# Kernel tuning notes

Measured on AMD Instinct MI355X. Metric: run time of the kernel, lower is better.

Reference implementation:

```python
import jax, jax.numpy as jnp
import numpy as np

N, E, H, D_IN, D_OUT, DEPTH, G = 100000, 1600000, 128, 128, 10, 3, 256


def setup_inputs() -> dict:
    key = jax.random.key(0)
    ks = jax.random.split(key, 16)
    s = lambda k, shape: jax.random.normal(k, shape, dtype=jnp.float32) * 0.05
    inp = {
        "x": jax.random.normal(ks[0], (N, D_IN), dtype=jnp.float32),
        "edge_index": jax.random.randint(ks[1], (2, E), 0, N, dtype=jnp.int32),
        "control_edge_index": jax.random.randint(ks[2], (2, 1024), 0, N, dtype=jnp.int32),
        "batch": jnp.sort(jax.random.randint(ks[3], (N,), 0, G, dtype=jnp.int32)),
        # encoder MLP: input_dim -> hidden -> hidden
        "enc_w1": s(ks[4], (D_IN, H)), "enc_b1": jnp.zeros((H,), jnp.float32),
        "enc_w2": s(ks[5], (H, H)),    "enc_b2": jnp.zeros((H,), jnp.float32),
        # conv_depth GCN layers, hidden -> hidden
        "conv_w": s(ks[6], (DEPTH, H, H)), "conv_b": jnp.zeros((DEPTH, H), jnp.float32),
        # decoder MLP: hidden -> hidden -> output_dim
        "dec_w1": s(ks[7], (H, H)),     "dec_b1": jnp.zeros((H,), jnp.float32),
        "dec_w2": s(ks[8], (H, D_OUT)), "dec_b2": jnp.zeros((D_OUT,), jnp.float32),
    }
    return inp


def _gcn_forward(x, enc_w1, enc_b1, enc_w2, enc_b2, conv_w, conv_b,
                 dec_w1, dec_b1, dec_w2, dec_b2, edge_index, batch):
    # encoder MLP (Linear-ReLU-Dropout(eval)-Linear)
    h = jax.nn.relu(x @ enc_w1 + enc_b1) @ enc_w2 + enc_b2

    # GCN normalization with self-loops: D^{-1/2} (A + I) D^{-1/2}
    loops = jnp.arange(N, dtype=edge_index.dtype)
    src = jnp.concatenate([edge_index[0], loops])  # [E + N]
    dst = jnp.concatenate([edge_index[1], loops])
    deg = jax.ops.segment_sum(jnp.ones_like(src, dtype=h.dtype), dst, num_segments=N)
    inv_sqrt = jax.lax.rsqrt(deg)  # deg >= 1 thanks to self-loops
    coef = (inv_sqrt[src] * inv_sqrt[dst])[:, None]  # [E+N, 1]

    for l in range(DEPTH):
        hw = h @ conv_w[l] + conv_b[l]                      # [N, H]
        h = jax.ops.segment_sum(hw[src] * coef, dst, num_segments=N)
        if l < DEPTH - 1:  # linear=False -> nonlinearity between convs
            h = jax.nn.relu(h)

    # global_add_pool over graph ids
    pooled = jax.ops.segment_sum(h, batch, num_segments=G)   # [G, H]

    # decoder MLP
    return jax.nn.relu(pooled @ dec_w1 + dec_b1) @ dec_w2 + dec_b2  # [G, D_OUT]


def reference(x, edge_index, control_edge_index, batch, enc_w1, enc_b1, enc_w2,
              enc_b2, conv_w, conv_b, dec_w1, dec_b1, dec_w2, dec_b2):
    # control_edge_index corresponds to the (disabled) control mechanism; unused
    return _gcn_forward(x, enc_w1, enc_b1, enc_w2, enc_b2, conv_w, conv_b,
                        dec_w1, dec_b1, dec_w2, dec_b2, edge_index, batch)
```

## Files before the change

### kernel.cpp

```cpp
#include <hip/hip_runtime.h>
#include <hip/hip_bf16.h>
#include <cstdint>
#include <cstddef>

#define NN 100000
#define NE 1600000
#define HH 128
#define NG 256

#define NB 196
#define BSH 9
#define BMSK 511
#define CHUNK 4096
#define NBLK 391
#define GB 782
#define NBK 391

typedef __bf16 bf16x8 __attribute__((ext_vector_type(8)));
typedef float floatx4 __attribute__((ext_vector_type(4)));

__device__ __forceinline__ uint32_t f2b(float f) {
  union { float f; uint32_t u; } v; v.f = f;
  uint32_t u = v.u;
  return (u + 0x7FFFu + ((u >> 16) & 1u)) >> 16;
}
__device__ __forceinline__ float blo(uint32_t u) {
  union { uint32_t u; float f; } v; v.u = u << 16;
  return v.f;
}
__device__ __forceinline__ float bhi(uint32_t u) {
  union { uint32_t u; float f; } v; v.u = u & 0xFFFF0000u;
  return v.f;
}
__device__ __forceinline__ void addrow(float* a, uint4 v) {
  a[0] += blo(v.x); a[1] += bhi(v.x);
  a[2] += blo(v.y); a[3] += bhi(v.y);
  a[4] += blo(v.z); a[5] += bhi(v.z);
  a[6] += blo(v.w); a[7] += bhi(v.w);
}

__device__ __forceinline__ void stage_w(uint16_t (*Wt)[136], const float* __restrict__ W,
                                        int tid) {
  for (int it = 0; it < 16; ++it) {
    int idx = tid + it * 256;
    int n = idx & 127;
    int k0 = (idx >> 7) * 4;
    uint2 wv;
    wv.x = f2b(W[(k0 + 0) * 128 + n]) | (f2b(W[(k0 + 1) * 128 + n]) << 16);
    wv.y = f2b(W[(k0 + 2) * 128 + n]) | (f2b(W[(k0 + 3) * 128 + n]) << 16);
    *(uint2*)&Wt[n][k0] = wv;
  }
}

__global__ __launch_bounds__(256) void k_front(const int* __restrict__ src,
                                               int* __restrict__ blkcnt,
                                               const float* __restrict__ conv_w,
                                               uint16_t* __restrict__ wbf,
                                               float* __restrict__ pooled) {
  int t = threadIdx.x;
  if (blockIdx.x < NBLK) {
    __shared__ int h[NB];
    if (t < NB) h[t] = 0;
    __syncthreads();
    int base = blockIdx.x * CHUNK, end = min(base + CHUNK, NE);
    for (int i = base + t; i < end; i += 256) atomicAdd(&h[src[i] >> BSH], 1);
    __syncthreads();
    if (t < NB) blkcnt[blockIdx.x * NB + t] = h[t];
  } else if (blockIdx.x < NBLK + 128) {
    int idx = (blockIdx.x - NBLK) * 256 + t;
    int l = idx >> 14;
    int n = (idx >> 7) & 127;
    int k = idx & 127;
    wbf[idx] = (uint16_t)f2b(conv_w[(l + 1) * 16384 + k * 128 + n]);
  } else {
    int i = ((blockIdx.x - NBLK - 128) * 256 + t) * 4;
    if (i < NG * HH) *(float4*)&pooled[i] = make_float4(0.f, 0.f, 0.f, 0.f);
  }
}

__global__ __launch_bounds__(256) void k_cntB(const uint2* __restrict__ pairs,
                                              int* __restrict__ blkcnt) {
  __shared__ int h[NB];
  int t = threadIdx.x;
  if (t < NB) h[t] = 0;
  __syncthreads();
  int base = blockIdx.x * CHUNK, end = min(base + CHUNK, NE);
  for (int i = base + t; i < end; i += 256) atomicAdd(&h[pairs[i].y >> BSH], 1);
  __syncthreads();
  if (t < NB) blkcnt[blockIdx.x * NB + t] = h[t];
}

__global__ void k_scan(const int* __restrict__ blkcnt, int* __restrict__ poff,
                       int* __restrict__ gbase, int* __restrict__ off, int set_off) {
  __shared__ int s[256];
  int t = threadIdx.x;
  int tot = 0;
  if (t < NB) {
    for (int r = 0; r < NBLK; ++r) {
      poff[r * NB + t] = tot;
      tot += blkcnt[r * NB + t];
    }
  }
  s[t] = (t < NB) ? tot : 0;
  __syncthreads();
  for (int d = 1; d < 256; d <<= 1) {
    int v = (t >= d) ? s[t - d] : 0;
    __syncthreads();
    s[t] += v;
    __syncthreads();
  }
  if (t < NB) gbase[t] = s[t] - tot;
  if (t == 0) { gbase[NB] = NE; if (set_off) off[NN] = NE; }
}

__global__ __launch_bounds__(256) void k_placeA(const int* __restrict__ src,
                                                const int* __restrict__ dst,
                                                const int* __restrict__ poff,
                                                const int* __restrict__ gbase,
                                                uint2* __restrict__ pairs) {
  __shared__ int cur[NB];
  int t = threadIdx.x;
  if (t < NB) cur[t] = poff[blockIdx.x * NB + t] + gbase[t];
  __syncthreads();
  int base = blockIdx.x * CHUNK, end = min(base + CHUNK, NE);
  for (int i = base + t; i < end; i += 256) {
    int s = src[i], d = dst[i];
    int p = atomicAdd(&cur[s >> BSH], 1);
    pairs[p] = make_uint2((unsigned)s, (unsigned)d);
  }
}

__global__ __launch_bounds__(256) void k_placeB(const uint2* __restrict__ pairs,
                                                const int* __restrict__ poff,
                                                const int* __restrict__ gbase,
                                                uint32_t* __restrict__ outb) {
  __shared__ int cur[NB];
  int t = threadIdx.x;
  if (t < NB) cur[t] = poff[blockIdx.x * NB + t] + gbase[t];
  __syncthreads();
  int base = blockIdx.x * CHUNK, end = min(base + CHUNK, NE);
  for (int i = base + t; i < end; i += 256) {
    uint2 v = pairs[i];
    int p = atomicAdd(&cur[v.y >> BSH], 1);
    outb[p] = v.x | ((v.y & (unsigned)BMSK) << 17);
  }
}

__global__ __launch_bounds__(256) void k_sortenc(
    const uint32_t* __restrict__ pairbuf, const int* __restrict__ gbase,
    const int* __restrict__ batch,
    int* __restrict__ off, int* __restrict__ csrs,
    int* __restrict__ dhist2, int* __restrict__ gstart,
    const float* __restrict__ A32, const float* __restrict__ W,
    const float* __restrict__ bias, uint16_t* __restrict__ Out)
{
  __shared__ char smraw[34816];
  const int tid = threadIdx.x;

  if (blockIdx.x < GB) {
    auto Wt = (uint16_t(*)[136])smraw;
    stage_w(Wt, W, tid);
    __syncthreads();

    const int lane = tid & 63;
    const int wave = tid >> 6;
    const int lrow = lane & 15;
    const int quad = lane >> 4;
    const int lk = quad * 8;
    const int row0 = blockIdx.x * 128 + wave * 32;

    floatx4 acc[2][8];
#pragma unroll
    for (int t = 0; t < 2; ++t)
#pragma unroll
      for (int n = 0; n < 8; ++n)
        acc[t][n] = (floatx4){0.f, 0.f, 0.f, 0.f};

#pragma unroll
    for (int ks = 0; ks < 4; ++ks) {
      bf16x8 a[2];
#pragma unroll
      for (int t = 0; t < 2; ++t) {
        int r = row0 + t * 16 + lrow;
        uint4 tmp = {0u, 0u, 0u, 0u};
        if (r < NN) {
          float4 f0 = *(const float4*)(A32 + (size_t)r * HH + ks * 32 + lk);
          float4 f1 = *(const float4*)(A32 + (size_t)r * HH + ks * 32 + lk + 4);
          tmp.x = f2b(f0.x) | (f2b(f0.y) << 16);
          tmp.y = f2b(f0.z) | (f2b(f0.w) << 16);
          tmp.z = f2b(f1.x) | (f2b(f1.y) << 16);
          tmp.w = f2b(f1.z) | (f2b(f1.w) << 16);
        }
        a[t] = __builtin_bit_cast(bf16x8, tmp);
      }
#pragma unroll
      for (int n = 0; n < 8; ++n) {
        bf16x8 b = __builtin_bit_cast(bf16x8, *(const uint4*)&Wt[n * 16 + lrow][ks * 32 + lk]);
        acc[0][n] = __builtin_amdgcn_mfma_f32_16x16x32_bf16(b, a[0], acc[0][n], 0, 0, 0);
        acc[1][n] = __builtin_amdgcn_mfma_f32_16x16x32_bf16(b, a[1], acc[1][n], 0, 0, 0);
      }
    }

    float4 b4[8];
#pragma unroll
    for (int n = 0; n < 8; ++n) b4[n] = *(const float4*)(bias + n * 16 + quad * 4);

#pragma unroll
    for (int t = 0; t < 2; ++t) {
      int row = row0 + t * 16 + lrow;
      if (row < NN) {
        uint16_t* orow = Out + (size_t)row * HH;
#pragma unroll
        for (int n = 0; n < 8; ++n) {
          float v0 = fmaxf(acc[t][n][0] + b4[n].x, 0.f);
          float v1 = fmaxf(acc[t][n][1] + b4[n].y, 0.f);
          float v2 = fmaxf(acc[t][n][2] + b4[n].z, 0.f);
          float v3 = fmaxf(acc[t][n][3] + b4[n].w, 0.f);
          uint2 o;
          o.x = f2b(v0) | (f2b(v1) << 16);
          o.y = f2b(v2) | (f2b(v3) << 16);
          *(uint2*)(orow + n * 16 + quad * 4) = o;
        }
      }
    }
  } else {
    int* cnt  = (int*)smraw;
    int* loff = cnt + 512;
    int* psum = loff + 512;
    int b = blockIdx.x - GB;
    cnt[tid] = 0; cnt[tid + 256] = 0;
    __syncthreads();
    int s0 = gbase[b], s1 = gbase[b + 1];
    for (int i = s0 + tid; i < s1; i += 256)
      atomicAdd(&cnt[pairbuf[i] >> 17], 1);
    __syncthreads();
    int a0 = cnt[2 * tid], a1 = cnt[2 * tid + 1];
    int s = a0 + a1;
    psum[tid] = s;
    __syncthreads();
    for (int d = 1; d < 256; d <<= 1) {
      int v = (tid >= d) ? psum[tid - d] : 0;
      __syncthreads();
      psum[tid] += v;
      __syncthreads();
    }
    int excl = psum[tid] - s;
    loff[2 * tid] = excl;
    loff[2 * tid + 1] = excl + a0;
    __syncthreads();
    int* h64 = psum;
    if (tid < 64) h64[tid] = 0;
    __syncthreads();
#pragma unroll
    for (int k = 0; k < 2; ++k) {
      int i = tid + k * 256;
      int node = b * 512 + i;
      if (node < NN) {
        off[node] = s0 + loff[i];
        int d = cnt[i]; if (d > 63) d = 63;
        atomicAdd(&h64[d], 1);
      }
    }
    {
      int n0 = b * 512, n1 = min(n0 + 512, NN);
      for (int i = n0 + tid; i < n1; i += 256) {
        int bb = batch[i];
        if (i == 0) { for (int g = 0; g <= bb; ++g) gstart[g] = 0; }
        else { int aa = batch[i - 1]; for (int g = aa + 1; g <= bb; ++g) gstart[g] = i; }
        if (i == NN - 1) { for (int g = bb + 1; g <= NG; ++g) gstart[g] = NN; }
      }
    }
    __syncthreads();
    if (tid < 64) dhist2[b * 64 + tid] = h64[tid];
    cnt[tid] = loff[tid]; cnt[tid + 256] = loff[tid + 256];
    __syncthreads();
    for (int i = s0 + tid; i < s1; i += 256) {
      uint32_t v = pairbuf[i];
      int p = atomicAdd(&cnt[v >> 17], 1);
      csrs[s0 + p] = (int)(v & 0x1FFFFu);
    }
  }
}

__global__ __launch_bounds__(256) void k_dinv(const int* __restrict__ dhist2,
                                              int* __restrict__ dcur,
                                              const int* __restrict__ off,
                                              float* __restrict__ inv) {
  if (blockIdx.x == 0) {
    int t = threadIdx.x;
    if (t < 64) {
      int sum = 0;
      for (int r = 0; r < NB; ++r) sum += dhist2[r * 64 + (63 - t)];
      int v = sum;
      for (int d = 1; d < 64; d <<= 1) { int u = __shfl_up(v, d); if (t >= d) v += u; }
      dcur[63 - t] = v - sum;
    }
  } else {
    int i = (blockIdx.x - 1) * 256 + threadIdx.x;
    if (i < NN) inv[i] = rsqrtf((float)(off[i + 1] - off[i]) + 1.0f);
  }
}

__global__ __launch_bounds__(256) void k_dualplace(
    const uint16_t* __restrict__ A16,
    const float* __restrict__ Wa, const float* __restrict__ ba,
    const float* __restrict__ Wb, const float* __restrict__ bb,
    const float* __restrict__ scale, uint16_t* __restrict__ Out,
    const int* __restrict__ off, int* __restrict__ dcur, int* __restrict__ order)
{
  __shared__ uint16_t Wt[128][136];
  __shared__ uint16_t tile[128][136];
  const int tid = threadIdx.x;

  if (blockIdx.x < GB) {
    stage_w(Wt, Wa, tid);
    __syncthreads();

    const int lane = tid & 63;
    const int wave = tid >> 6;
    const int lrow = lane & 15;
    const int quad = lane >> 4;
    const int lk = quad * 8;
    const int row0 = blockIdx.x * 128 + wave * 32;
    const int trow0 = wave * 32;

    floatx4 acc[2][8];
#pragma unroll
    for (int t = 0; t < 2; ++t)
#pragma unroll
      for (int n = 0; n < 8; ++n)
        acc[t][n] = (floatx4){0.f, 0.f, 0.f, 0.f};

#pragma unroll
    for (int ks = 0; ks < 4; ++ks) {
      bf16x8 a[2];
#pragma unroll
      for (int t = 0; t < 2; ++t) {
        int r = row0 + t * 16 + lrow;
        uint4 tmp = {0u, 0u, 0u, 0u};
        if (r < NN) tmp = *(const uint4*)(A16 + (size_t)r * HH + ks * 32 + lk);
        a[t] = __builtin_bit_cast(bf16x8, tmp);
      }
#pragma unroll
      for (int n = 0; n < 8; ++n) {
        bf16x8 b = __builtin_bit_cast(bf16x8, *(const uint4*)&Wt[n * 16 + lrow][ks * 32 + lk]);
        acc[0][n] = __builtin_amdgcn_mfma_f32_16x16x32_bf16(b, a[0], acc[0][n], 0, 0, 0);
        acc[1][n] = __builtin_amdgcn_mfma_f32_16x16x32_bf16(b, a[1], acc[1][n], 0, 0, 0);
      }
    }

    {
      float4 b4[8];
#pragma unroll
      for (int n = 0; n < 8; ++n) b4[n] = *(const float4*)(ba + n * 16 + quad * 4);
#pragma unroll
      for (int t = 0; t < 2; ++t) {
        int trow = trow0 + t * 16 + lrow;
#pragma unroll
        for (int n = 0; n < 8; ++n) {
          uint2 o;
          o.x = f2b(acc[t][n][0] + b4[n].x) | (f2b(acc[t][n][1] + b4[n].y) << 16);
          o.y = f2b(acc[t][n][2] + b4[n].z) | (f2b(acc[t][n][3] + b4[n].w) << 16);
          *(uint2*)&tile[trow][n * 16 + quad * 4] = o;
        }
      }
    }
    __syncthreads();
    stage_w(Wt, Wb, tid);
#pragma unroll
    for (int t = 0; t < 2; ++t)
#pragma unroll
      for (int n = 0; n < 8; ++n)
        acc[t][n] = (floatx4){0.f, 0.f, 0.f, 0.f};
    __syncthreads();

#pragma unroll
    for (int ks = 0; ks < 4; ++ks) {
      bf16x8 a[2];
#pragma unroll
      for (int t = 0; t < 2; ++t)
        a[t] = __builtin_bit_cast(bf16x8,
                 *(const uint4*)&tile[trow0 + t * 16 + lrow][ks * 32 + lk]);
#pragma unroll
      for (int n = 0; n < 8; ++n) {
        bf16x8 b = __builtin_bit_cast(bf16x8, *(const uint4*)&Wt[n * 16 + lrow][ks * 32 + lk]);
        acc[0][n] = __builtin_amdgcn_mfma_f32_16x16x32_bf16(b, a[0], acc[0][n], 0, 0, 0);
        acc[1][n] = __builtin_amdgcn_mfma_f32_16x16x32_bf16(b, a[1], acc[1][n], 0, 0, 0);
      }
    }

    {
      float4 b4[8];
#pragma unroll
      for (int n = 0; n < 8; ++n) b4[n] = *(const float4*)(bb + n * 16 + quad * 4);
#pragma unroll
      for (int t = 0; t < 2; ++t) {
        int row = row0 + t * 16 + lrow;
        if (row < NN) {
          float sc = scale[row];
          uint16_t* orow = Out + (size_t)row * HH;
#pragma unroll
          for (int n = 0; n < 8; ++n) {
            float v0 = (acc[t][n][0] + b4[n].x) * sc;
            float v1 = (acc[t][n][1] + b4[n].y) * sc;
            float v2 = (acc[t][n][2] + b4[n].z) * sc;
            float v3 = (acc[t][n][3] + b4[n].w) * sc;
            uint2 o;
            o.x = f2b(v0) | (f2b(v1) << 16);
            o.y = f2b(v2) | (f2b(v3) << 16);
            *(uint2*)(orow + n * 16 + quad * 4) = o;
          }
        }
      }
    }
  } else {
    int* h = (int*)Wt;
    int* base = h + 64;
    if (tid < 64) h[tid] = 0;
    __syncthreads();
    int i = (blockIdx.x - GB) * 256 + tid;
    int d = 0, ld = 0;
    if (i < NN) { d = off[i + 1] - off[i]; if (d > 63) d = 63; ld = atomicAdd(&h[d], 1); }
    __syncthreads();
    if (tid < 64) base[tid] = h[tid] ? atomicAdd(&dcur[tid], h[tid]) : 0;
    __syncthreads();
    if (i < NN) order[base[d] + ld] = i;
  }
}

__global__ __launch_bounds__(512) void k_aggemm(
    const uint16_t* __restrict__ hw2, const int* __restrict__ off,
    const int* __restrict__ csrs, const float* __restrict__ inv,
    const int* __restrict__ order,
    const uint16_t* __restrict__ Wbf, const float* __restrict__ bias,
    uint16_t* __restrict__ Out)
{
  __shared__ uint4 S4[32][16];
  __shared__ int nid[32];
  const int tid = threadIdx.x;
  const int lane = tid & 63;
  const int wave = tid >> 6;
  const int lrow = lane & 15;
  const int quad = lane >> 4;
  const int lk = quad * 8;

  const uint16_t* wrow = Wbf + (size_t)(wave * 16 + lrow) * HH;
  uint4 w0 = *(const uint4*)(wrow + 0 * 32 + lk);
  uint4 w1 = *(const uint4*)(wrow + 1 * 32 + lk);
  uint4 w2 = *(const uint4*)(wrow + 2 * 32 + lk);
  uint4 w3 = *(const uint4*)(wrow + 3 * 32 + lk);

  const int group = tid >> 4;
  const int node = order[blockIdx.x * 32 + group];
  const int c = (tid & 15) * 8;
  if ((tid & 15) == 0) nid[group] = node;
  const uint16_t* rowp = hw2 + c;

  uint4 sv = *(const uint4*)(rowp + (size_t)node * HH);
  float a[8] = {0.f, 0.f, 0.f, 0.f, 0.f, 0.f, 0.f, 0.f};
  addrow(a, sv);

  int e0 = off[node], e1 = off[node + 1];
  int e = e0;
  for (; e + 4 <= e1; e += 4) {
    int s0 = csrs[e + 0], s1 = csrs[e + 1], s2 = csrs[e + 2], s3 = csrs[e + 3];
    uint4 v0 = *(const uint4*)(rowp + (size_t)s0 * HH);
    uint4 v1 = *(const uint4*)(rowp + (size_t)s1 * HH);
    uint4 v2 = *(const uint4*)(rowp + (size_t)s2 * HH);
    uint4 v3 = *(const uint4*)(rowp + (size_t)s3 * HH);
    addrow(a, v0); addrow(a, v1); addrow(a, v2); addrow(a, v3);
  }
  for (; e < e1; ++e) {
    int s = csrs[e];
    uint4 v = *(const uint4*)(rowp + (size_t)s * HH);
    addrow(a, v);
  }
  float invd = inv[node];
#pragma unroll
  for (int j = 0; j < 8; ++j) a[j] = fmaxf(a[j] * invd, 0.f);
  {
    uint4 o;
    o.x = f2b(a[0]) | (f2b(a[1]) << 16);
    o.y = f2b(a[2]) | (f2b(a[3]) << 16);
    o.z = f2b(a[4]) | (f2b(a[5]) << 16);
    o.w = f2b(a[6]) | (f2b(a[7]) << 16);
    S4[group][(tid & 15) ^ (group & 15)] = o;
  }
  __syncthreads();

  floatx4 acc0 = (floatx4){0.f, 0.f, 0.f, 0.f};
  floatx4 acc1 = (floatx4){0.f, 0.f, 0.f, 0.f};
#pragma unroll
  for (int ks = 0; ks < 4; ++ks) {
    int ch = (ks * 4 + quad) ^ lrow;
    bf16x8 a0 = __builtin_bit_cast(bf16x8, S4[lrow][ch]);
    bf16x8 a1 = __builtin_bit_cast(bf16x8, S4[16 + lrow][ch]);
    uint4 wv = (ks == 0) ? w0 : (ks == 1) ? w1 : (ks == 2) ? w2 : w3;
    bf16x8 b  = __builtin_bit_cast(bf16x8, wv);
    acc0 = __builtin_amdgcn_mfma_f32_16x16x32_bf16(b, a0, acc0, 0, 0, 0);
    acc1 = __builtin_amdgcn_mfma_f32_16x16x32_bf16(b, a1, acc1, 0, 0, 0);
  }

  float4 b4 = *(const float4*)(bias + wave * 16 + quad * 4);
#pragma unroll
  for (int t = 0; t < 2; ++t) {
    floatx4 ac = t ? acc1 : acc0;
    int row = nid[t * 16 + lrow];
    float sc = inv[row];
    float v0 = (ac[0] + b4.x) * sc;
    float v1 = (ac[1] + b4.y) * sc;
    float v2 = (ac[2] + b4.z) * sc;
    float v3 = (ac[3] + b4.w) * sc;
    uint2 o;
    o.x = f2b(v0) | (f2b(v1) << 16);
    o.y = f2b(v2) | (f2b(v3) << 16);
    *(uint2*)(Out + (size_t)row * HH + wave * 16 + quad * 4) = o;
  }
}

__global__ __launch_bounds__(256) void k_aggpool(
    const uint16_t* __restrict__ hw2, const int* __restrict__ off,
    const int* __restrict__ csrs, const float* __restrict__ inv,
    const int* __restrict__ batch,
    float* __restrict__ pooled)
{
  __shared__ float red[16][132];
  __shared__ int gid[16];
  const int tid = threadIdx.x;
  const int slot = tid >> 4;
  const int node = blockIdx.x * 16 + slot;
  const int c = (tid & 15) * 8;
  if ((tid & 15) == 0) gid[slot] = batch[node];
  const uint16_t* rowp = hw2 + c;

  uint4 sv = *(const uint4*)(rowp + (size_t)node * HH);
  float a[8] = {0.f, 0.f, 0.f, 0.f, 0.f, 0.f, 0.f, 0.f};
  addrow(a, sv);

  int e0 = off[node], e1 = off[node + 1];
  int e = e0;
  for (; e + 4 <= e1; e += 4) {
    int s0 = csrs[e + 0], s1 = csrs[e + 1], s2 = csrs[e + 2], s3 = csrs[e + 3];
    uint4 v0 = *(const uint4*)(rowp + (size_t)s0 * HH);
    uint4 v1 = *(const uint4*)(rowp + (size_t)s1 * HH);
    uint4 v2 = *(const uint4*)(rowp + (size_t)s2 * HH);
    uint4 v3 = *(const uint4*)(rowp + (size_t)s3 * HH);
    addrow(a, v0); addrow(a, v1); addrow(a, v2); addrow(a, v3);
  }
  for (; e < e1; ++e) {
    int s = csrs[e];
    uint4 v = *(const uint4*)(rowp + (size_t)s * HH);
    addrow(a, v);
  }
  float invd = inv[node];
#pragma unroll
  for (int j = 0; j < 8; ++j) a[j] *= invd;
  *(float4*)&red[slot][c]     = make_float4(a[0], a[1], a[2], a[3]);
  *(float4*)&red[slot][c + 4] = make_float4(a[4], a[5], a[6], a[7]);
  __syncthreads();

  if (tid < 128) {
    int g = gid[0];
    float run = red[0][tid];
    for (int r = 1; r < 16; ++r) {
      int gg = gid[r];
      if (gg != g) {
        unsafeAtomicAdd(&pooled[(size_t)g * HH + tid], run);
        run = 0.f; g = gg;
      }
      run += red[r][tid];
    }
    unsafeAtomicAdd(&pooled[(size_t)g * HH + tid], run);
  }
}

__global__ __launch_bounds__(256) void k_dec(
    const float* __restrict__ pooled,
    const float* __restrict__ w1, const float* __restrict__ b1,
    const float* __restrict__ w2, const float* __restrict__ b2,
    float* __restrict__ out)
{
  __shared__ float p[128], tmpv[128];
  int g = blockIdx.x;
  int tid = threadIdx.x;
  if (tid < 128) p[tid] = pooled[(size_t)g * HH + tid];
  __syncthreads();
  if (tid < 128) {
    float acc1 = b1[tid];
    for (int k = 0; k < 128; ++k) acc1 += p[k] * w1[k * 128 + tid];
    tmpv[tid] = fmaxf(acc1, 0.f);
  }
  __syncthreads();
  if (tid < 10) {
    float o = b2[tid];
    for (int k = 0; k < 128; ++k) o += tmpv[k] * w2[k * 10 + tid];
    out[g * 10 + tid] = o;
  }
}

extern "C" void kernel_launch(void* const* d_in, const int* in_sizes, int n_in,
                              void* d_out, int out_size, void* d_ws, size_t ws_size,
                              hipStream_t stream) {
  const float* x       = (const float*)d_in[0];
  const int*   eidx    = (const int*)d_in[1];
  const int*   src     = eidx;
  const int*   dst     = eidx + NE;
  const int*   batch   = (const int*)d_in[3];
  const float* enc_w1  = (const float*)d_in[4];
  const float* enc_b1  = (const float*)d_in[5];
  const float* enc_w2  = (const float*)d_in[6];
  const float* enc_b2  = (const float*)d_in[7];
  const float* conv_w  = (const float*)d_in[8];
  const float* conv_b  = (const float*)d_in[9];
  const float* dec_w1  = (const float*)d_in[10];
  const float* dec_b1  = (const float*)d_in[11];
  const float* dec_w2  = (const float*)d_in[12];
  const float* dec_b2  = (const float*)d_in[13];
  float* out = (float*)d_out;

  char* ws = (char*)d_ws;
  size_t o = 0;
  auto alloc = [&](size_t bytes) -> char* {
    char* p = ws + o;
    o += (bytes + 255) & ~(size_t)255;
    return p;
  };
  int*      off     = (int*)alloc((size_t)(NN + 1) * 4);
  int*      csrs    = (int*)alloc((size_t)NE * 4);
  float*    inv     = (float*)alloc((size_t)NN * 4);
  int*      blkcntA = (int*)alloc((size_t)NBLK * NB * 4);
  int*      poffA   = (int*)alloc((size_t)NBLK * NB * 4);
  int*      blkcntB = (int*)alloc((size_t)NBLK * NB * 4);
  int*      poffB   = (int*)alloc((size_t)NBLK * NB * 4);
  int*      gbaseA  = (int*)alloc((size_t)(NB + 1) * 4);
  int*      gbaseB  = (int*)alloc((size_t)(NB + 1) * 4);
  int*      dhist2  = (int*)alloc((size_t)NB * 64 * 4);
  int*      dcur    = (int*)alloc(64 * 4);
  int*      order   = (int*)alloc((size_t)NN * 4);
  int*      gstart  = (int*)alloc((size_t)(NG + 1) * 4);
  float*    pooled  = (float*)alloc((size_t)NG * HH * 4);
  uint16_t* wbf     = (uint16_t*)alloc((size_t)2 * 16384 * 2);
  uint32_t* pairB   = (uint32_t*)alloc((size_t)NE * 4);
  uint16_t* buf0    = (uint16_t*)alloc((size_t)NN * HH * 2);
  uint16_t* buf1    = (uint16_t*)alloc((size_t)NN * HH * 2);
  uint2*    pairsA  = (uint2*)buf1;

  k_front<<<dim3(NBLK + 128 + 32), dim3(256), 0, stream>>>(src, blkcntA, conv_w, wbf, pooled);
  k_scan<<<dim3(1), dim3(256), 0, stream>>>(blkcntA, poffA, gbaseA, off, 0);
  k_placeA<<<dim3(NBLK), dim3(256), 0, stream>>>(src, dst, poffA, gbaseA, pairsA);
  k_cntB<<<dim3(NBLK), dim3(256), 0, stream>>>(pairsA, blkcntB);
  k_scan<<<dim3(1), dim3(256), 0, stream>>>(blkcntB, poffB, gbaseB, off, 1);
  k_placeB<<<dim3(NBLK), dim3(256), 0, stream>>>(pairsA, poffB, gbaseB, pairB);
  k_sortenc<<<dim3(GB + NB), dim3(256), 0, stream>>>(pairB, gbaseB, batch, off, csrs,
                                                     dhist2, gstart,
                                                     x, enc_w1, enc_b1, buf1);
  k_dinv<<<dim3(1 + NBK), dim3(256), 0, stream>>>(dhist2, dcur, off, inv);
  k_dualplace<<<dim3(GB + NBK), dim3(256), 0, stream>>>(buf1, enc_w2, enc_b2,
                                                        conv_w + 0 * 16384, conv_b + 0,
                                                        inv, buf0, off, dcur, order);

  const int FB = NN / 32;
  const int AB = NN / 16;
  k_aggemm<<<dim3(FB), dim3(512), 0, stream>>>(buf0, off, csrs, inv, order,
                                               wbf, conv_b + 128, buf1);
  k_aggemm<<<dim3(FB), dim3(512), 0, stream>>>(buf1, off, csrs, inv, order,
                                               wbf + 16384, conv_b + 256, buf0);
  k_aggpool<<<dim3(AB), dim3(256), 0, stream>>>(buf0, off, csrs, inv, batch, pooled);

  k_dec<<<dim3(NG), dim3(256), 0, stream>>>(pooled, dec_w1, dec_b1, dec_w2, dec_b2, out);
}
```

Measured before the change: 485.2 us.

## Fuse second-pass histogram into placeA via global atomics and transpose block counts

Drops the separate k_cntB pass over the 12.8MB pairs buffer. k_placeA now bumps the destination-bucket histogram per output chunk with global atomics, and the new zeroing blocks in k_front clear that histogram first. Block-count arrays are transposed to column-major so the single-block k_scan reads each column contiguously with 8-way unrolled loads. k_aggemm now loads the weight fragments after the gather phase instead of holding them in registers, which lowers register pressure. The cost is 1.6M global atomics on a 76K-entry array.

```diff
diff --git a/kernel.cpp b/kernel.cpp
--- a/kernel.cpp
+++ b/kernel.cpp
@@ -12,9 +12,11 @@
 #define BSH 9
 #define BMSK 511
 #define CHUNK 4096
+#define CSH 12
 #define NBLK 391
 #define GB 782
 #define NBK 391
+#define NBZ 300
 
 typedef __bf16 bf16x8 __attribute__((ext_vector_type(8)));
 typedef float floatx4 __attribute__((ext_vector_type(4)));
@@ -53,7 +55,8 @@
 }
 
 __global__ __launch_bounds__(256) void k_front(const int* __restrict__ src,
-                                               int* __restrict__ blkcnt,
+                                               int* __restrict__ blkcntA,
+                                               int* __restrict__ blkcntB,
                                                const float* __restrict__ conv_w,
                                                uint16_t* __restrict__ wbf,
                                                float* __restrict__ pooled) {
@@ -65,29 +68,20 @@
     int base = blockIdx.x * CHUNK, end = min(base + CHUNK, NE);
     for (int i = base + t; i < end; i += 256) atomicAdd(&h[src[i] >> BSH], 1);
     __syncthreads();
-    if (t < NB) blkcnt[blockIdx.x * NB + t] = h[t];
+    if (t < NB) blkcntA[t * NBLK + blockIdx.x] = h[t];
   } else if (blockIdx.x < NBLK + 128) {
     int idx = (blockIdx.x - NBLK) * 256 + t;
     int l = idx >> 14;
     int n = (idx >> 7) & 127;
     int k = idx & 127;
     wbf[idx] = (uint16_t)f2b(conv_w[(l + 1) * 16384 + k * 128 + n]);
-  } else {
+  } else if (blockIdx.x < NBLK + 128 + 32) {
     int i = ((blockIdx.x - NBLK - 128) * 256 + t) * 4;
     if (i < NG * HH) *(float4*)&pooled[i] = make_float4(0.f, 0.f, 0.f, 0.f);
-  }
-}
-
-__global__ __launch_bounds__(256) void k_cntB(const uint2* __restrict__ pairs,
-                                              int* __restrict__ blkcnt) {
-  __shared__ int h[NB];
-  int t = threadIdx.x;
-  if (t < NB) h[t] = 0;
-  __syncthreads();
-  int base = blockIdx.x * CHUNK, end = min(base + CHUNK, NE);
-  for (int i = base + t; i < end; i += 256) atomicAdd(&h[pairs[i].y >> BSH], 1);
-  __syncthreads();
-  if (t < NB) blkcnt[blockIdx.x * NB + t] = h[t];
+  } else {
+    int i = (blockIdx.x - NBLK - 160) * 256 + t;
+    if (i < NB * NBLK) blkcntB[i] = 0;
+  }
 }
 
 __global__ void k_scan(const int* __restrict__ blkcnt, int* __restrict__ poff,
@@ -96,10 +90,17 @@
   int t = threadIdx.x;
   int tot = 0;
   if (t < NB) {
-    for (int r = 0; r < NBLK; ++r) {
-      poff[r * NB + t] = tot;
-      tot += blkcnt[r * NB + t];
-    }
+    const int* col = blkcnt + (size_t)t * NBLK;
+    int* pcol = poff + (size_t)t * NBLK;
+    int r0 = 0;
+    for (; r0 + 8 <= NBLK; r0 += 8) {
+      int v[8];
+#pragma unroll
+      for (int j = 0; j < 8; ++j) v[j] = col[r0 + j];
+#pragma unroll
+      for (int j = 0; j < 8; ++j) { pcol[r0 + j] = tot; tot += v[j]; }
+    }
+    for (; r0 < NBLK; ++r0) { pcol[r0] = tot; tot += col[r0]; }
   }
   s[t] = (t < NB) ? tot : 0;
   __syncthreads();
@@ -117,16 +118,18 @@
                                                 const int* __restrict__ dst,
                                                 const int* __restrict__ poff,
                                                 const int* __restrict__ gbase,
-                                                uint2* __restrict__ pairs) {
+                                                uint2* __restrict__ pairs,
+                                                int* __restrict__ blkcntB) {
   __shared__ int cur[NB];
   int t = threadIdx.x;
-  if (t < NB) cur[t] = poff[blockIdx.x * NB + t] + gbase[t];
+  if (t < NB) cur[t] = poff[(size_t)t * NBLK + blockIdx.x] + gbase[t];
   __syncthreads();
   int base = blockIdx.x * CHUNK, end = min(base + CHUNK, NE);
   for (int i = base + t; i < end; i += 256) {
     int s = src[i], d = dst[i];
     int p = atomicAdd(&cur[s >> BSH], 1);
     pairs[p] = make_uint2((unsigned)s, (unsigned)d);
+    atomicAdd(&blkcntB[(d >> BSH) * NBLK + (p >> CSH)], 1);
   }
 }
 
@@ -136,7 +139,7 @@
                                                 uint32_t* __restrict__ outb) {
   __shared__ int cur[NB];
   int t = threadIdx.x;
-  if (t < NB) cur[t] = poff[blockIdx.x * NB + t] + gbase[t];
+  if (t < NB) cur[t] = poff[(size_t)t * NBLK + blockIdx.x] + gbase[t];
   __syncthreads();
   int base = blockIdx.x * CHUNK, end = min(base + CHUNK, NE);
   for (int i = base + t; i < end; i += 256) {
@@ -438,17 +441,6 @@
   __shared__ uint4 S4[32][16];
   __shared__ int nid[32];
   const int tid = threadIdx.x;
-  const int lane = tid & 63;
-  const int wave = tid >> 6;
-  const int lrow = lane & 15;
-  const int quad = lane >> 4;
-  const int lk = quad * 8;
-
-  const uint16_t* wrow = Wbf + (size_t)(wave * 16 + lrow) * HH;
-  uint4 w0 = *(const uint4*)(wrow + 0 * 32 + lk);
-  uint4 w1 = *(const uint4*)(wrow + 1 * 32 + lk);
-  uint4 w2 = *(const uint4*)(wrow + 2 * 32 + lk);
-  uint4 w3 = *(const uint4*)(wrow + 3 * 32 + lk);
 
   const int group = tid >> 4;
   const int node = order[blockIdx.x * 32 + group];
@@ -488,6 +480,13 @@
   }
   __syncthreads();
 
+  const int lane = tid & 63;
+  const int wave = tid >> 6;
+  const int lrow = lane & 15;
+  const int quad = lane >> 4;
+  const int lk = quad * 8;
+  const uint16_t* wrow = Wbf + (size_t)(wave * 16 + lrow) * HH;
+
   floatx4 acc0 = (floatx4){0.f, 0.f, 0.f, 0.f};
   floatx4 acc1 = (floatx4){0.f, 0.f, 0.f, 0.f};
 #pragma unroll
@@ -495,8 +494,7 @@
     int ch = (ks * 4 + quad) ^ lrow;
     bf16x8 a0 = __builtin_bit_cast(bf16x8, S4[lrow][ch]);
     bf16x8 a1 = __builtin_bit_cast(bf16x8, S4[16 + lrow][ch]);
-    uint4 wv = (ks == 0) ? w0 : (ks == 1) ? w1 : (ks == 2) ? w2 : w3;
-    bf16x8 b  = __builtin_bit_cast(bf16x8, wv);
+    bf16x8 b  = __builtin_bit_cast(bf16x8, *(const uint4*)(wrow + ks * 32 + lk));
     acc0 = __builtin_amdgcn_mfma_f32_16x16x32_bf16(b, a0, acc0, 0, 0, 0);
     acc1 = __builtin_amdgcn_mfma_f32_16x16x32_bf16(b, a1, acc1, 0, 0, 0);
   }
@@ -645,10 +643,10 @@
   uint16_t* buf1    = (uint16_t*)alloc((size_t)NN * HH * 2);
   uint2*    pairsA  = (uint2*)buf1;
 
-  k_front<<<dim3(NBLK + 128 + 32), dim3(256), 0, stream>>>(src, blkcntA, conv_w, wbf, pooled);
+  k_front<<<dim3(NBLK + 128 + 32 + NBZ), dim3(256), 0, stream>>>(src, blkcntA, blkcntB,
+                                                                 conv_w, wbf, pooled);
   k_scan<<<dim3(1), dim3(256), 0, stream>>>(blkcntA, poffA, gbaseA, off, 0);
-  k_placeA<<<dim3(NBLK), dim3(256), 0, stream>>>(src, dst, poffA, gbaseA, pairsA);
-  k_cntB<<<dim3(NBLK), dim3(256), 0, stream>>>(pairsA, blkcntB);
+  k_placeA<<<dim3(NBLK), dim3(256), 0, stream>>>(src, dst, poffA, gbaseA, pairsA, blkcntB);
   k_scan<<<dim3(1), dim3(256), 0, stream>>>(blkcntB, poffB, gbaseB, off, 1);
   k_placeB<<<dim3(NBLK), dim3(256), 0, stream>>>(pairsA, poffB, gbaseB, pairB);
   k_sortenc<<<dim3(GB + NB), dim3(256), 0, stream>>>(pairB, gbaseB, batch, off, csrs,
```

Measured after the change: 529.4 us. 1.09x slower.
